# Kernel optimization log

Hardware: AMD Instinct MI355X
Metric: run time of the kernel (lower is better)

## Reference

```python
import jax, jax.numpy as jnp
import numpy as np

B, S, D, H = 2, 2048, 1024, 16
DK = D // H  # 64


def rotate_half(x):
    d = x.shape[-1]
    x1, x2 = x[..., : d // 2], x[..., d // 2 :]
    return jnp.concatenate([-x2, x1], axis=-1)


def apply_rope(q, k):
    # q, k: [B, H, S, DK]
    d_k = q.shape[-1]
    seq_len = q.shape[-2]
    theta = 10000.0 ** (-2.0 / d_k * jnp.arange(d_k // 2, dtype=q.dtype))
    positions = jnp.arange(seq_len, dtype=q.dtype)
    angles = jnp.outer(positions, theta)                    # [S, DK/2]
    cos = jnp.tile(jnp.cos(angles), (1, 2))                 # [S, DK]
    sin = jnp.tile(jnp.sin(angles), (1, 2))
    q = q * cos + rotate_half(q) * sin
    k = k * cos + rotate_half(k) * sin
    return q, k


def setup_inputs() -> dict:
    key = jax.random.key(0)
    ks = jax.random.split(key, 9)
    std = 1.0 / np.sqrt(D)
    x = jax.random.normal(ks[0], (B, S, D), dtype=jnp.float32)
    # mask True = masked (code uses masked_fill(mask, -inf)); causal mask
    mask = jnp.triu(jnp.ones((S, S), dtype=bool), k=1)[None, None, :, :]
    mask = jnp.broadcast_to(mask, (B, 1, S, S))
    Wq = jax.random.uniform(ks[1], (D, D), jnp.float32, -std, std)
    bq = jax.random.uniform(ks[2], (D,), jnp.float32, -std, std)
    Wk = jax.random.uniform(ks[3], (D, D), jnp.float32, -std, std)
    bk = jax.random.uniform(ks[4], (D,), jnp.float32, -std, std)
    Wv = jax.random.uniform(ks[5], (D, D), jnp.float32, -std, std)
    bv = jax.random.uniform(ks[6], (D,), jnp.float32, -std, std)
    Wo = jax.random.uniform(ks[7], (D, D), jnp.float32, -std, std)
    bo = jax.random.uniform(ks[8], (D,), jnp.float32, -std, std)
    return {"x": x, "mask": mask, "Wq": Wq, "bq": bq, "Wk": Wk, "bk": bk,
            "Wv": Wv, "bv": bv, "Wo": Wo, "bo": bo}


def reference(x, mask, Wq, bq, Wk, bk, Wv, bv, Wo, bo):
    b, s, d = x.shape
    # projections -> [B, H, S, DK]
    q = (x @ Wq + bq).reshape(b, s, H, DK).transpose(0, 2, 1, 3)
    k = (x @ Wk + bk).reshape(b, s, H, DK).transpose(0, 2, 1, 3)
    v = (x @ Wv + bv).reshape(b, s, H, DK).transpose(0, 2, 1, 3)
    q, k = apply_rope(q, k)
    scores = jnp.einsum("bhqd,bhkd->bhqk", q, k) / np.sqrt(DK)
    scores = jnp.where(mask, -jnp.inf, scores)
    probs = jax.nn.softmax(scores, axis=-1)
    attn = jnp.einsum("bhqk,bhkd->bhqd", probs, v)
    o = attn.transpose(0, 2, 1, 3).reshape(b, s, H * DK)
    return o @ Wo + bo
```

## Files before the change

### kernel.cpp

```cpp
#include <hip/hip_runtime.h>
#include <hip/hip_bf16.h>
#include <math.h>

typedef __hip_bfloat16 bf16;
typedef __attribute__((ext_vector_type(8))) short short8;
typedef __attribute__((ext_vector_type(4))) short s16x4;
typedef __attribute__((ext_vector_type(4))) float f32x4;

#define B_  2
#define S_  2048
#define D_  1024
#define H_  16
#define DK_ 64

#define QSCALE 0.18033688011112043f
#define EXPOFF 11.541560327111707f

__device__ inline short bfs(float f) { return __builtin_bit_cast(short, __float2bfloat16(f)); }

#define GLL16(gptr, lptr)                                                        \
    __builtin_amdgcn_global_load_lds(                                            \
        (const __attribute__((address_space(1))) void*)(gptr),                   \
        (__attribute__((address_space(3))) void*)(lptr), 16, 0, 0)

#if __has_builtin(__builtin_amdgcn_mfma_f32_16x16x16bf16_1k)
#define MFMA_16x16x16(A, Bv, C) __builtin_amdgcn_mfma_f32_16x16x16bf16_1k(A, Bv, C, 0, 0, 0)
#elif __has_builtin(__builtin_amdgcn_mfma_f32_16x16x16_bf16)
#define MFMA_16x16x16(A, Bv, C) __builtin_amdgcn_mfma_f32_16x16x16_bf16(A, Bv, C, 0, 0, 0)
#else
static __device__ inline f32x4 mfma16_asm(s16x4 a, s16x4 b, f32x4 c) {
    f32x4 d;
    asm volatile("v_mfma_f32_16x16x16_bf16 %0, %1, %2, %3\n\ts_nop 7\n\ts_nop 7"
                 : "=v"(d) : "v"(a), "v"(b), "v"(c));
    return d;
}
#define MFMA_16x16x16(A, Bv, C) mfma16_asm(A, Bv, C)
#endif

__global__ __launch_bounds__(256)
void prep_k(const float* __restrict__ x,
            const float* __restrict__ W0, const float* __restrict__ W1,
            const float* __restrict__ W2, const float* __restrict__ W3,
            bf16* __restrict__ cx, bf16* __restrict__ Wt)
{
    const int z = blockIdx.z;
    const int t = threadIdx.x;
    if (z == 4) {
        const int bid = blockIdx.y * 16 + blockIdx.x;
        #pragma unroll
        for (int i = 0; i < 16; i++) {
            const size_t g = ((size_t)bid * 256 + t) * 4 + (size_t)i * 262144;
            const float4 v = *(const float4*)(x + g);
            s16x4 o = { bfs(v.x), bfs(v.y), bfs(v.z), bfs(v.w) };
            *(s16x4*)(cx + g) = o;
        }
        return;
    }
    __shared__ float Lt[64][65];
    const float* W = (z == 0) ? W0 : (z == 1) ? W1 : (z == 2) ? W2 : W3;
    bf16* dst = Wt + (size_t)z * D_ * D_;
    const int k0 = blockIdx.y * 64, n0 = blockIdx.x * 64;
    #pragma unroll
    for (int p = 0; p < 4; p++) {
        const int idx = p * 256 + t;
        const int row = idx >> 4, cb = (idx & 15) * 4;
        const float4 v = *(const float4*)(W + (size_t)(k0 + row) * D_ + n0 + cb);
        Lt[cb + 0][row] = v.x; Lt[cb + 1][row] = v.y;
        Lt[cb + 2][row] = v.z; Lt[cb + 3][row] = v.w;
    }
    __syncthreads();
    #pragma unroll
    for (int p = 0; p < 4; p++) {
        const int idx = p * 256 + t;
        const int n = idx >> 4, kb = (idx & 15) * 4;
        s16x4 o = { bfs(Lt[n][kb]), bfs(Lt[n][kb + 1]), bfs(Lt[n][kb + 2]), bfs(Lt[n][kb + 3]) };
        *(s16x4*)(dst + (size_t)(n0 + n) * D_ + k0 + kb) = o;
    }
}

template<int MODE, int TM>
__global__ __launch_bounds__(256)
void gemm_k(const bf16* __restrict__ A, const bf16* __restrict__ WtAll,
            const float* __restrict__ b0, const float* __restrict__ b1,
            const float* __restrict__ b2,
            bf16* __restrict__ d0, bf16* __restrict__ d1, bf16* __restrict__ d2,
            float* __restrict__ fout)
{
    constexpr int K = D_;
    constexpr int MT = (B_ * S_) / TM;
    constexpr int AI = TM / 64;
    const int L = (int)blockIdx.x;
    const int m0 = (L & (MT - 1)) * TM;
    const int rest = L / MT;
    const int z = (MODE == 0) ? (rest >> 4) : 3;
    const int n0 = (MODE == 0) ? (rest & 15) * 64 : rest * 64;
    const bf16* W = WtAll + (size_t)z * D_ * D_;
    const float* bias = (MODE == 1) ? b0 : ((z == 0) ? b0 : (z == 1) ? b1 : b2);

    __shared__ __align__(16) short As[TM * 32];
    __shared__ __align__(16) short Bs[64 * 32];

    const int t = threadIdx.x;
    const int wave = t >> 6, lane = t & 63, quad = lane >> 4, l16 = lane & 15;
    const int wm = wave * (TM / 4);

    const bf16* gA0 = A + (size_t)(m0 + (t >> 2)) * K + (t & 3) * 8;
    const bf16* gA1 = gA0 + (size_t)64 * K;
    const bf16* gW0 = W + (size_t)(n0 + (t >> 2)) * K + (t & 3) * 8;
    const int wb = wave * 512;

    f32x4 acc[AI][4] = {};

    for (int k0 = 0; k0 < K; k0 += 32) {
        __syncthreads();
        GLL16(gA0 + k0, &As[wb]);
        if (TM == 128) GLL16(gA1 + k0, &As[2048 + wb]);
        GLL16(gW0 + k0, &Bs[wb]);
        __syncthreads();
        short8 af[AI], bf[4];
        #pragma unroll
        for (int i = 0; i < AI; i++) af[i] = *(const short8*)&As[(wm + i * 16 + l16) * 32 + quad * 8];
        #pragma unroll
        for (int j = 0; j < 4; j++) bf[j] = *(const short8*)&Bs[(j * 16 + l16) * 32 + quad * 8];
        #pragma unroll
        for (int i = 0; i < AI; i++)
            #pragma unroll
            for (int j = 0; j < 4; j++)
                acc[i][j] = __builtin_amdgcn_mfma_f32_16x16x32_bf16(af[i], bf[j], acc[i][j], 0, 0, 0);
    }

    if (MODE == 1) {
        #pragma unroll
        for (int j = 0; j < 4; j++) {
            const int ncol = n0 + j * 16 + l16;
            const float bb = bias[ncol];
            #pragma unroll
            for (int i = 0; i < AI; i++) {
                const int mbase = m0 + wm + i * 16 + quad * 4;
                #pragma unroll
                for (int r = 0; r < 4; r++)
                    fout[(size_t)(mbase + r) * D_ + ncol] = acc[i][j][r] + bb;
            }
        }
    } else if (z == 2) {
        const int h = n0 >> 6;
        #pragma unroll
        for (int j = 0; j < 4; j++) {
            const int ncol = n0 + j * 16 + l16;
            const float bb = bias[ncol];
            const int dk = ncol & 63;
            #pragma unroll
            for (int i = 0; i < AI; i++) {
                const int mbase = m0 + wm + i * 16 + quad * 4;
                #pragma unroll
                for (int r = 0; r < 4; r++) {
                    const int m = mbase + r;
                    const int b = m >> 11, s = m & (S_ - 1);
                    d2[(((size_t)(b * H_ + h)) * DK_ + dk) * S_ + s] = __float2bfloat16(acc[i][j][r] + bb);
                }
            }
        }
    } else {
        bf16* dst = z ? d1 : d0;
        const float sc = z ? 1.0f : QSCALE;
        const int h = n0 >> 6;
        #pragma unroll
        for (int j = 0; j < 2; j++) {
            const int dk = j * 16 + l16;
            const float th = exp2f((float)dk * -0.41524101186092029f);
            const float blo = bias[(h << 6) + dk];
            const float bhi = bias[(h << 6) + dk + 32];
            #pragma unroll
            for (int i = 0; i < AI; i++) {
                #pragma unroll
                for (int r = 0; r < 4; r++) {
                    const int m = m0 + wm + i * 16 + quad * 4 + r;
                    const int b = m >> 11, s = m & (S_ - 1);
                    float sn, cs;
                    sincosf((float)s * th, &sn, &cs);
                    const float v1 = acc[i][j][r] + blo;
                    const float v2 = acc[i][j + 2][r] + bhi;
                    bf16* p = dst + (((size_t)(b * H_ + h)) * S_ + s) * DK_;
                    p[dk]      = __float2bfloat16((v1 * cs - v2 * sn) * sc);
                    p[dk + 32] = __float2bfloat16((v2 * cs + v1 * sn) * sc);
                }
            }
        }
    }
}

__device__ __forceinline__
void attn_tile(const short* __restrict__ Ks, const short* __restrict__ Vts,
               const short8 qf0, const short8 qf1,
               f32x4* ot, float& l_acc,
               const bool diag, const int wave, const int quad, const int l16)
{
    const int kkmax = diag ? wave : 3;
    for (int kk = 0; kk <= kkmax; kk++) {
        const short8 kf0 = *(const short8*)&Ks[(kk * 16 + l16) * 72 + quad * 8];
        const short8 kf1 = *(const short8*)&Ks[(kk * 16 + l16) * 72 + 32 + quad * 8];
        f32x4 st = {};
        st = __builtin_amdgcn_mfma_f32_16x16x32_bf16(kf0, qf0, st, 0, 0, 0);
        st = __builtin_amdgcn_mfma_f32_16x16x32_bf16(kf1, qf1, st, 0, 0, 0);

        s16x4 pt;
        float psum = 0.0f;
        #pragma unroll
        for (int r = 0; r < 4; r++) {
            const bool masked = diag && (kk == wave) && (quad * 4 + r > l16);
            const float p = masked ? 0.0f : exp2f(st[r] - EXPOFF);
            psum += p;
            pt[r] = bfs(p);
        }
        l_acc += psum;

        #pragma unroll
        for (int dt = 0; dt < 4; dt++) {
            const s16x4 vf = *(const s16x4*)&Vts[(dt * 16 + l16) * 72 + kk * 16 + quad * 4];
            ot[dt] = MFMA_16x16x16(vf, pt, ot[dt]);
        }
    }
}

__global__ __launch_bounds__(256)
void attn_k(const bf16* __restrict__ q_ws, const bf16* __restrict__ k_ws,
            const bf16* __restrict__ vt_ws, bf16* __restrict__ attn_ws)
{
    __shared__ __align__(16) short Ks[64 * 72];
    __shared__ __align__(16) short Vts[64 * 72];

    const int bh = (int)blockIdx.x;
    const int qt = 31 - (int)blockIdx.y;
    const int q0 = qt * 64;
    const int t = threadIdx.x;
    const int wave = t >> 6, quad = (t & 63) >> 4, l16 = t & 15;
    const bf16* Kb = k_ws + (size_t)bh * S_ * DK_;
    const bf16* Vb = vt_ws + (size_t)bh * DK_ * S_;
    const int b = bh >> 4, h = bh & 15;

    const bf16* Qb = q_ws + ((size_t)bh * S_ + q0 + wave * 16) * DK_;
    const short8 qf0 = *(const short8*)(Qb + (size_t)l16 * DK_ + quad * 8);
    const short8 qf1 = *(const short8*)(Qb + (size_t)l16 * DK_ + 32 + quad * 8);

    float l_acc = 0.0f;
    f32x4 ot[4] = {};

    for (int kt = 0; kt <= qt; kt++) {
        __syncthreads();
        #pragma unroll
        for (int p = 0; p < 2; p++) {
            const int idx = p * 256 + t;
            const int row = idx >> 3, cb = (idx & 7) * 8;
            *(float4*)&Ks[row * 72 + cb]  = *(const float4*)(Kb + (size_t)(kt * 64 + row) * DK_ + cb);
            *(float4*)&Vts[row * 72 + cb] = *(const float4*)(Vb + (size_t)row * S_ + kt * 64 + cb);
        }
        __syncthreads();

        attn_tile(Ks, Vts, qf0, qf1, ot, l_acc, kt == qt, wave, quad, l16);
    }

    l_acc += __shfl_xor(l_acc, 16, 64);
    l_acc += __shfl_xor(l_acc, 32, 64);
    const float inv = 1.0f / l_acc;
    const int srow = q0 + wave * 16 + l16;
    bf16* orow = attn_ws + ((size_t)(b * S_ + srow)) * D_ + h * 64;
    #pragma unroll
    for (int dt = 0; dt < 4; dt++) {
        s16x4 o4 = { bfs(ot[dt][0] * inv), bfs(ot[dt][1] * inv),
                     bfs(ot[dt][2] * inv), bfs(ot[dt][3] * inv) };
        *(s16x4*)(orow + dt * 16 + quad * 4) = o4;
    }
}

extern "C" void kernel_launch(void* const* d_in, const int* in_sizes, int n_in,
                              void* d_out, int out_size, void* d_ws, size_t ws_size,
                              hipStream_t stream)
{
    (void)out_size; (void)ws_size;
    const float* x = nullptr;
    const float* W[4] = {nullptr, nullptr, nullptr, nullptr};
    const float* bias[4] = {nullptr, nullptr, nullptr, nullptr};
    int wi = 0, bi = 0;
    for (int i = 0; i < n_in; i++) {
        const int sz = in_sizes[i];
        if (sz == B_ * S_ * D_ && x == nullptr) x = (const float*)d_in[i];
        else if (sz == D_ * D_ && wi < 4) W[wi++] = (const float*)d_in[i];
        else if (sz == D_ && bi < 4) bias[bi++] = (const float*)d_in[i];
    }

    bf16* ws = (bf16*)d_ws;
    const size_t SEG = (size_t)B_ * S_ * D_;
    bf16* canonX  = ws;
    bf16* Wt      = ws + SEG;
    bf16* k_ws    = ws + 2 * SEG;
    bf16* vt_ws   = ws + 3 * SEG;
    bf16* attn_ws = canonX;
    bf16* q_ws    = (bf16*)d_out;

    prep_k<<<dim3(16, 16, 5), 256, 0, stream>>>(x, W[0], W[1], W[2], W[3], canonX, Wt);

    gemm_k<0, 128><<<dim3(1536, 1, 1), 256, 0, stream>>>(
        canonX, Wt, bias[0], bias[1], bias[2], q_ws, k_ws, vt_ws, nullptr);

    attn_k<<<dim3(32, 32), 256, 0, stream>>>(q_ws, k_ws, vt_ws, attn_ws);

    gemm_k<1, 64><<<dim3(1024, 1, 1), 256, 0, stream>>>(
        attn_ws, Wt, bias[3], nullptr, nullptr, nullptr, nullptr, nullptr,
        (float*)d_out);
}
```

Before: 242.1 us.

## Pair causal query tiles per block and load two KV tiles per sync

Each attention block now handles two query tiles, qt and 31-qt, which balances causal work across blocks and lets both tiles reuse every K/V tile staged in shared memory. K/V staging is double-width, with two 64-row tiles loaded between barriers, which halves the number of syncs. The tile function is templated on whether it is a diagonal tile so the masking branch drops out of off-diagonal tiles, and its inner loop is unrolled. The grid shrinks to 512 blocks and register and LDS use per block roughly doubles, which may lower occupancy.

```diff
diff --git a/kernel.cpp b/kernel.cpp
--- a/kernel.cpp
+++ b/kernel.cpp
@@ -189,13 +189,15 @@
     }
 }
 
+template<bool DIAG>
 __device__ __forceinline__
 void attn_tile(const short* __restrict__ Ks, const short* __restrict__ Vts,
                const short8 qf0, const short8 qf1,
                f32x4* ot, float& l_acc,
-               const bool diag, const int wave, const int quad, const int l16)
-{
-    const int kkmax = diag ? wave : 3;
+               const int wave, const int quad, const int l16)
+{
+    const int kkmax = DIAG ? wave : 3;
+    #pragma unroll
     for (int kk = 0; kk <= kkmax; kk++) {
         const short8 kf0 = *(const short8*)&Ks[(kk * 16 + l16) * 72 + quad * 8];
         const short8 kf1 = *(const short8*)&Ks[(kk * 16 + l16) * 72 + 32 + quad * 8];
@@ -207,8 +209,13 @@
         float psum = 0.0f;
         #pragma unroll
         for (int r = 0; r < 4; r++) {
-            const bool masked = diag && (kk == wave) && (quad * 4 + r > l16);
-            const float p = masked ? 0.0f : exp2f(st[r] - EXPOFF);
+            float p;
+            if (DIAG) {
+                const bool masked = (kk == wave) && (quad * 4 + r > l16);
+                p = masked ? 0.0f : exp2f(st[r] - EXPOFF);
+            } else {
+                p = exp2f(st[r] - EXPOFF);
+            }
             psum += p;
             pt[r] = bfs(p);
         }
@@ -226,49 +233,83 @@
 void attn_k(const bf16* __restrict__ q_ws, const bf16* __restrict__ k_ws,
             const bf16* __restrict__ vt_ws, bf16* __restrict__ attn_ws)
 {
-    __shared__ __align__(16) short Ks[64 * 72];
-    __shared__ __align__(16) short Vts[64 * 72];
-
-    const int bh = (int)blockIdx.x;
-    const int qt = 31 - (int)blockIdx.y;
-    const int q0 = qt * 64;
+    __shared__ __align__(16) short Ks[2][64 * 72];
+    __shared__ __align__(16) short Vts[2][64 * 72];
+
+    const int linear = (int)blockIdx.y * 16 + (int)blockIdx.x;
+    const int bh = linear & 31;
+    const int pr = linear >> 5;
+    const int qtA = pr, qtB = 31 - pr;
     const int t = threadIdx.x;
     const int wave = t >> 6, quad = (t & 63) >> 4, l16 = t & 15;
     const bf16* Kb = k_ws + (size_t)bh * S_ * DK_;
     const bf16* Vb = vt_ws + (size_t)bh * DK_ * S_;
     const int b = bh >> 4, h = bh & 15;
 
-    const bf16* Qb = q_ws + ((size_t)bh * S_ + q0 + wave * 16) * DK_;
-    const short8 qf0 = *(const short8*)(Qb + (size_t)l16 * DK_ + quad * 8);
-    const short8 qf1 = *(const short8*)(Qb + (size_t)l16 * DK_ + 32 + quad * 8);
-
-    float l_acc = 0.0f;
-    f32x4 ot[4] = {};
-
-    for (int kt = 0; kt <= qt; kt++) {
+    const bf16* QbA = q_ws + ((size_t)bh * S_ + qtA * 64 + wave * 16) * DK_;
+    const bf16* QbB = q_ws + ((size_t)bh * S_ + qtB * 64 + wave * 16) * DK_;
+    const short8 qfA0 = *(const short8*)(QbA + (size_t)l16 * DK_ + quad * 8);
+    const short8 qfA1 = *(const short8*)(QbA + (size_t)l16 * DK_ + 32 + quad * 8);
+    const short8 qfB0 = *(const short8*)(QbB + (size_t)l16 * DK_ + quad * 8);
+    const short8 qfB1 = *(const short8*)(QbB + (size_t)l16 * DK_ + 32 + quad * 8);
+
+    float lA = 0.0f, lB = 0.0f;
+    f32x4 otA[4] = {}, otB[4] = {};
+
+    for (int kt0 = 0; kt0 <= qtB; kt0 += 2) {
+        const int kt1 = kt0 + 1;
+        const bool has1 = (kt1 <= qtB);
         __syncthreads();
         #pragma unroll
         for (int p = 0; p < 2; p++) {
             const int idx = p * 256 + t;
             const int row = idx >> 3, cb = (idx & 7) * 8;
-            *(float4*)&Ks[row * 72 + cb]  = *(const float4*)(Kb + (size_t)(kt * 64 + row) * DK_ + cb);
-            *(float4*)&Vts[row * 72 + cb] = *(const float4*)(Vb + (size_t)row * S_ + kt * 64 + cb);
+            *(float4*)&Ks[0][row * 72 + cb]  = *(const float4*)(Kb + (size_t)(kt0 * 64 + row) * DK_ + cb);
+            *(float4*)&Vts[0][row * 72 + cb] = *(const float4*)(Vb + (size_t)row * S_ + kt0 * 64 + cb);
+        }
+        if (has1) {
+            #pragma unroll
+            for (int p = 0; p < 2; p++) {
+                const int idx = p * 256 + t;
+                const int row = idx >> 3, cb = (idx & 7) * 8;
+                *(float4*)&Ks[1][row * 72 + cb]  = *(const float4*)(Kb + (size_t)(kt1 * 64 + row) * DK_ + cb);
+                *(float4*)&Vts[1][row * 72 + cb] = *(const float4*)(Vb + (size_t)row * S_ + kt1 * 64 + cb);
+            }
         }
         __syncthreads();
 
-        attn_tile(Ks, Vts, qf0, qf1, ot, l_acc, kt == qt, wave, quad, l16);
-    }
-
-    l_acc += __shfl_xor(l_acc, 16, 64);
-    l_acc += __shfl_xor(l_acc, 32, 64);
-    const float inv = 1.0f / l_acc;
-    const int srow = q0 + wave * 16 + l16;
-    bf16* orow = attn_ws + ((size_t)(b * S_ + srow)) * D_ + h * 64;
+        if (kt0 == qtB) attn_tile<true >(Ks[0], Vts[0], qfB0, qfB1, otB, lB, wave, quad, l16);
+        else            attn_tile<false>(Ks[0], Vts[0], qfB0, qfB1, otB, lB, wave, quad, l16);
+        if (has1) {
+            if (kt1 == qtB) attn_tile<true >(Ks[1], Vts[1], qfB0, qfB1, otB, lB, wave, quad, l16);
+            else            attn_tile<false>(Ks[1], Vts[1], qfB0, qfB1, otB, lB, wave, quad, l16);
+        }
+        if (kt0 <= qtA) {
+            if (kt0 == qtA) attn_tile<true >(Ks[0], Vts[0], qfA0, qfA1, otA, lA, wave, quad, l16);
+            else            attn_tile<false>(Ks[0], Vts[0], qfA0, qfA1, otA, lA, wave, quad, l16);
+        }
+        if (has1 && kt1 <= qtA) {
+            if (kt1 == qtA) attn_tile<true >(Ks[1], Vts[1], qfA0, qfA1, otA, lA, wave, quad, l16);
+            else            attn_tile<false>(Ks[1], Vts[1], qfA0, qfA1, otA, lA, wave, quad, l16);
+        }
+    }
+
     #pragma unroll
-    for (int dt = 0; dt < 4; dt++) {
-        s16x4 o4 = { bfs(ot[dt][0] * inv), bfs(ot[dt][1] * inv),
-                     bfs(ot[dt][2] * inv), bfs(ot[dt][3] * inv) };
-        *(s16x4*)(orow + dt * 16 + quad * 4) = o4;
+    for (int which = 0; which < 2; which++) {
+        float l_acc = which ? lB : lA;
+        f32x4* ot = which ? otB : otA;
+        const int q0 = (which ? qtB : qtA) * 64;
+        l_acc += __shfl_xor(l_acc, 16, 64);
+        l_acc += __shfl_xor(l_acc, 32, 64);
+        const float inv = 1.0f / l_acc;
+        const int srow = q0 + wave * 16 + l16;
+        bf16* orow = attn_ws + ((size_t)(b * S_ + srow)) * D_ + h * 64;
+        #pragma unroll
+        for (int dt = 0; dt < 4; dt++) {
+            s16x4 o4 = { bfs(ot[dt][0] * inv), bfs(ot[dt][1] * inv),
+                         bfs(ot[dt][2] * inv), bfs(ot[dt][3] * inv) };
+            *(s16x4*)(orow + dt * 16 + quad * 4) = o4;
+        }
     }
 }
 
@@ -302,7 +343,7 @@
     gemm_k<0, 128><<<dim3(1536, 1, 1), 256, 0, stream>>>(
         canonX, Wt, bias[0], bias[1], bias[2], q_ws, k_ws, vt_ws, nullptr);
 
-    attn_k<<<dim3(32, 32), 256, 0, stream>>>(q_ws, k_ws, vt_ws, attn_ws);
+    attn_k<<<dim3(16, 32), 256, 0, stream>>>(q_ws, k_ws, vt_ws, attn_ws);
 
     gemm_k<1, 64><<<dim3(1024, 1, 1), 256, 0, stream>>>(
         attn_ws, Wt, bias[3], nullptr, nullptr, nullptr, nullptr, nullptr,
```

Measured after the change: 217.5 us. 1.11x faster.
